# Performance work log

Hardware: AMD Instinct MI355X
Metric: run time of the kernel (lower is better)

Reference implementation:

```python
import jax, jax.numpy as jnp
import numpy as np

NUM_TNETS = 8388608
NUM_PINS = 20971520
NUM_NODES = 1048576

def setup_inputs() -> dict:
    key = jax.random.key(0)
    k1, k2, k3 = jax.random.split(key, 3)
    beta = jax.random.uniform(k1, (1,), dtype=jnp.float32)
    tnet_weights = jax.random.uniform(k2, (NUM_TNETS,), dtype=jnp.float32)
    flat_tnet2pin = jax.random.randint(k3, (2 * NUM_TNETS,), 0, NUM_PINS, dtype=jnp.int64)
    pin2node_map = jax.random.randint(jax.random.fold_in(key, 7), (NUM_PINS,), 0, NUM_NODES, dtype=jnp.int64)
    return {
        "beta": beta,
        "tnet_weights": tnet_weights,
        "flat_tnet2pin": flat_tnet2pin,
        "pin2node_map": pin2node_map,
    }

def reference(beta, tnet_weights, flat_tnet2pin, pin2node_map):
    # flat_tnet2pin layout: [src_0, dst_0, src_1, dst_1, ...] (2 pins per timing arc)
    # gather node id for every arc pin: [2*num_tnets]
    node_idx = pin2node_map[flat_tnet2pin]
    # each arc's weight is added at both its source and sink node
    w = jnp.repeat(tnet_weights, 2)  # [w0, w0, w1, w1, ...] matches flat layout
    out = jnp.zeros(NUM_NODES, dtype=jnp.float32).at[node_idx].add(w)
    return out * beta
```

## Files before the change

kernel.cpp:

```cpp
#include <hip/hip_runtime.h>
#include <stdint.h>


#define TILE 4096
#define THREADS 512
#define IPT  8
#define NB1  160
#define SHIFT1 17
#define CAP1 114688
#define TILES_PER_BIN1 28
#define NB2  256
#define SHIFT2 12
#define CAP2 81920
#define ACC_NODES 4096
#define CTRL_BYTES 8192

typedef unsigned long long item_t;
typedef int   int4_ev   __attribute__((ext_vector_type(4)));
typedef float float4_ev __attribute__((ext_vector_type(4)));
typedef unsigned long long ull2_ev __attribute__((ext_vector_type(2)));

__device__ __forceinline__ item_t pack_item(uint32_t key, float w) {
    return (item_t)key | ((item_t)__float_as_uint(w) << 32);
}

__device__ __forceinline__ void multisplit_flush(
    uint32_t (&key)[IPT], float (&wv)[IPT], int (&bin)[IPT],
    int tile_cnt, int shift,
    int* __restrict__ gcur, item_t* __restrict__ gout, size_t cap)
{
    __shared__ int hist[256];
    __shared__ int basex[256];
    __shared__ int gbase[256];
    __shared__ int wsum[4];
    __shared__ item_t stage[TILE];
    const int t = threadIdx.x;

    if (t < 256) hist[t] = 0;
    __syncthreads();

    int rank[IPT];
#pragma unroll
    for (int k = 0; k < IPT; ++k)
        rank[k] = (bin[k] >= 0) ? atomicAdd(&hist[bin[k]], 1) : 0;
    __syncthreads();

    int val = (t < 256) ? hist[t] : 0;
    int inc = val;
#pragma unroll
    for (int d = 1; d < 64; d <<= 1) {
        int n = __shfl_up(inc, d, 64);
        if ((t & 63) >= d) inc += n;
    }
    if (t < 256 && (t & 63) == 63) wsum[t >> 6] = inc;
    __syncthreads();
    if (t < 256) {
        int w = t >> 6, prefix = 0;
        if (w > 0) prefix += wsum[0];
        if (w > 1) prefix += wsum[1];
        if (w > 2) prefix += wsum[2];
        basex[t] = prefix + inc - val;
        gbase[t] = (val > 0) ? atomicAdd(&gcur[t], val) : 0;
    }
    __syncthreads();

#pragma unroll
    for (int k = 0; k < IPT; ++k) {
        if (bin[k] >= 0)
            stage[basex[bin[k]] + rank[k]] = pack_item(key[k], wv[k]);
    }
    __syncthreads();

    for (int j = t; j < tile_cnt; j += THREADS) {
        item_t e = stage[j];
        int b = (int)((uint32_t)(e & 0xffffffffull) >> shift);
        long long dst = (long long)gbase[b] + (j - basex[b]);
        if (dst >= 0 && dst < (long long)cap)
            __builtin_nontemporal_store(e, &gout[(size_t)b * cap + (size_t)dst]);
    }
}

__global__ __launch_bounds__(THREADS, 8) void k1_partition_pins(
    const int* __restrict__ flat_pins, const float* __restrict__ weights,
    int* __restrict__ cur1, item_t* __restrict__ items1, int total)
{
    const int tileBase = blockIdx.x * TILE;
    const int t = threadIdx.x;
    const int base = tileBase + t * IPT;
    uint32_t key[IPT]; float wv[IPT]; int bin[IPT];

    if (base + IPT <= total) {
        int4_ev   p[2];
        float4_ev w;
#pragma unroll
        for (int v = 0; v < 2; ++v)
            p[v] = __builtin_nontemporal_load((const int4_ev*)(flat_pins + base) + v);
        w = __builtin_nontemporal_load((const float4_ev*)(weights + (base >> 1)));
#pragma unroll
        for (int k = 0; k < IPT; ++k) {
            int pin = p[k >> 2][k & 3];
            key[k] = (uint32_t)pin;
            wv[k]  = w[(k >> 1) & 3];
            bin[k] = pin >> SHIFT1;
        }
    } else {
#pragma unroll
        for (int k = 0; k < IPT; ++k) {
            int i = base + k;
            bool ok = i < total;
            int pin = ok ? flat_pins[i] : 0;
            key[k] = (uint32_t)pin;
            wv[k]  = ok ? weights[i >> 1] : 0.f;
            bin[k] = ok ? (pin >> SHIFT1) : -1;
        }
    }
    int cnt = min(TILE, total - tileBase);
    multisplit_flush(key, wv, bin, cnt, SHIFT1, cur1, items1, (size_t)CAP1);
}

__global__ __launch_bounds__(THREADS, 8) void k2_gather_partition(
    const item_t* __restrict__ items1, const int* __restrict__ cur1,
    const int* __restrict__ pin2node,
    int* __restrict__ cur2, item_t* __restrict__ items2)
{
    const int q = blockIdx.x;
    const int r = q & 7;
    const int s = q >> 3;
    const int bin  = r + 8 * (s / TILES_PER_BIN1);
    const int tile = s % TILES_PER_BIN1;
    const int cnt = min(cur1[bin], (int)CAP1);
    const int tbase = tile * TILE;
    if (tbase >= cnt) return;

    const item_t* src = items1 + (size_t)bin * CAP1;
    const int t = threadIdx.x;
    const int base = tbase + t * IPT;
    uint32_t key[IPT]; float wv[IPT]; int b2[IPT];

    if (base + IPT <= cnt) {
        ull2_ev it[4];
#pragma unroll
        for (int v = 0; v < 4; ++v)
            it[v] = __builtin_nontemporal_load((const ull2_ev*)(src + base) + v);
#pragma unroll
        for (int k = 0; k < IPT; ++k) {
            item_t e = it[k >> 1][k & 1];
            int node = pin2node[(uint32_t)(e & 0xffffffffull)];
            key[k] = (uint32_t)node;
            wv[k]  = __uint_as_float((uint32_t)(e >> 32));
            b2[k]  = node >> SHIFT2;
        }
    } else {
#pragma unroll
        for (int k = 0; k < IPT; ++k) {
            int i = base + k;
            bool ok = i < cnt;
            item_t e = ok ? src[i] : 0ull;
            int node = ok ? pin2node[(uint32_t)(e & 0xffffffffull)] : 0;
            key[k] = (uint32_t)node;
            wv[k]  = __uint_as_float((uint32_t)(e >> 32));
            b2[k]  = ok ? (node >> SHIFT2) : -1;
        }
    }
    int tcnt = min(TILE, cnt - tbase);
    multisplit_flush(key, wv, b2, tcnt, SHIFT2, cur2, items2, (size_t)CAP2);
}

__global__ __launch_bounds__(1024) void k3_accumulate(
    const item_t* __restrict__ items2, const int* __restrict__ cur2,
    const float* __restrict__ beta, float* __restrict__ out, int num_nodes)
{
    __shared__ float acc[ACC_NODES];
    const int b = blockIdx.x;
    const int t = threadIdx.x;
    for (int i = t; i < ACC_NODES; i += 1024) acc[i] = 0.f;
    __syncthreads();
    const int cnt = min(cur2[b], (int)CAP2);
    const item_t* src = items2 + (size_t)b * CAP2;
    for (int i = t; i < cnt; i += 1024) {
        item_t it = __builtin_nontemporal_load(&src[i]);
        atomicAdd(&acc[(uint32_t)(it & 0xffffffffull) & (ACC_NODES - 1)],
                  __uint_as_float((uint32_t)(it >> 32)));
    }
    __syncthreads();
    const float bt = beta[0];
    const int nodeBase = b << SHIFT2;
    for (int i = t; i < ACC_NODES; i += 1024) {
        int n = nodeBase + i;
        if (n < num_nodes) out[n] = acc[i] * bt;
    }
}

__global__ __launch_bounds__(256) void scatter_device(
    const float* __restrict__ beta, const float* __restrict__ tnet_weights,
    const long long* __restrict__ pin_pairs, const int* __restrict__ pin2node_map,
    float* __restrict__ out, int num_tnets)
{
    int t = blockIdx.x * blockDim.x + threadIdx.x;
    if (t >= num_tnets) return;
    long long pp = pin_pairs[t];
    float w = tnet_weights[t] * beta[0];
    atomicAdd(&out[pin2node_map[(int)(pp & 0xffffffffLL)]], w);
    atomicAdd(&out[pin2node_map[(int)(pp >> 32)]], w);
}

extern "C" void kernel_launch(void* const* d_in, const int* in_sizes, int n_in,
                              void* d_out, int out_size, void* d_ws, size_t ws_size,
                              hipStream_t stream) {
    const float* beta         = (const float*)d_in[0];
    const float* weights      = (const float*)d_in[1];
    const int*   flat_pins    = (const int*)d_in[2];
    const int*   pin2node     = (const int*)d_in[3];
    float* out = (float*)d_out;

    const int num_tnets = in_sizes[1];
    const int total     = in_sizes[2];
    const int num_nodes = out_size;

    const size_t items1Bytes = (size_t)NB1 * CAP1 * sizeof(item_t);
    const size_t items2Bytes = (size_t)NB2 * CAP2 * sizeof(item_t);

    int* cur1 = (int*)d_ws;
    int* cur2 = (int*)((char*)d_ws + 2048);
    const int gridTiles = (total + TILE - 1) / TILE;

    if (ws_size >= CTRL_BYTES + items1Bytes + items2Bytes) {
        item_t* items1 = (item_t*)((char*)d_ws + CTRL_BYTES);
        item_t* items2 = (item_t*)((char*)d_ws + CTRL_BYTES + items1Bytes);
        (void)hipMemsetAsync(d_ws, 0, CTRL_BYTES, stream);
        k1_partition_pins<<<gridTiles, THREADS, 0, stream>>>(
            flat_pins, weights, cur1, items1, total);
        k2_gather_partition<<<NB1 * TILES_PER_BIN1, THREADS, 0, stream>>>(
            items1, cur1, pin2node, cur2, items2);
        k3_accumulate<<<NB2, 1024, 0, stream>>>(items2, cur2, beta, out, num_nodes);
    } else {
        (void)hipMemsetAsync(d_out, 0, (size_t)out_size * sizeof(float), stream);
        scatter_device<<<(num_tnets + 255) / 256, 256, 0, stream>>>(
            beta, weights, (const long long*)flat_pins, pin2node, out, num_tnets);
    }
}
```

Before: 483.6 us.

## Replace second partition pass with per-XCD global atomic partial sums

```diff
diff --git a/kernel.cpp b/kernel.cpp
--- a/kernel.cpp
+++ b/kernel.cpp
@@ -9,10 +9,7 @@
 #define SHIFT1 17
 #define CAP1 114688
 #define TILES_PER_BIN1 28
-#define NB2  256
-#define SHIFT2 12
-#define CAP2 81920
-#define ACC_NODES 4096
+#define NXCD 8
 #define CTRL_BYTES 8192
 
 typedef unsigned long long item_t;
@@ -118,10 +115,10 @@
     multisplit_flush(key, wv, bin, cnt, SHIFT1, cur1, items1, (size_t)CAP1);
 }
 
-__global__ __launch_bounds__(THREADS, 8) void k2_gather_partition(
+__global__ __launch_bounds__(THREADS, 8) void k2_gather_atomic(
     const item_t* __restrict__ items1, const int* __restrict__ cur1,
     const int* __restrict__ pin2node,
-    int* __restrict__ cur2, item_t* __restrict__ items2)
+    float* __restrict__ part, int num_nodes)
 {
     const int q = blockIdx.x;
     const int r = q & 7;
@@ -132,10 +129,10 @@
     const int tbase = tile * TILE;
     if (tbase >= cnt) return;
 
+    float* __restrict__ dst = part + (size_t)r * (size_t)num_nodes;
     const item_t* src = items1 + (size_t)bin * CAP1;
     const int t = threadIdx.x;
     const int base = tbase + t * IPT;
-    uint32_t key[IPT]; float wv[IPT]; int b2[IPT];
 
     if (base + IPT <= cnt) {
         ull2_ev it[4];
@@ -146,48 +143,45 @@
         for (int k = 0; k < IPT; ++k) {
             item_t e = it[k >> 1][k & 1];
             int node = pin2node[(uint32_t)(e & 0xffffffffull)];
-            key[k] = (uint32_t)node;
-            wv[k]  = __uint_as_float((uint32_t)(e >> 32));
-            b2[k]  = node >> SHIFT2;
+            atomicAdd(&dst[node], __uint_as_float((uint32_t)(e >> 32)));
         }
     } else {
 #pragma unroll
         for (int k = 0; k < IPT; ++k) {
             int i = base + k;
-            bool ok = i < cnt;
-            item_t e = ok ? src[i] : 0ull;
-            int node = ok ? pin2node[(uint32_t)(e & 0xffffffffull)] : 0;
-            key[k] = (uint32_t)node;
-            wv[k]  = __uint_as_float((uint32_t)(e >> 32));
-            b2[k]  = ok ? (node >> SHIFT2) : -1;
-        }
-    }
-    int tcnt = min(TILE, cnt - tbase);
-    multisplit_flush(key, wv, b2, tcnt, SHIFT2, cur2, items2, (size_t)CAP2);
-}
-
-__global__ __launch_bounds__(1024) void k3_accumulate(
-    const item_t* __restrict__ items2, const int* __restrict__ cur2,
-    const float* __restrict__ beta, float* __restrict__ out, int num_nodes)
-{
-    __shared__ float acc[ACC_NODES];
-    const int b = blockIdx.x;
-    const int t = threadIdx.x;
-    for (int i = t; i < ACC_NODES; i += 1024) acc[i] = 0.f;
-    __syncthreads();
-    const int cnt = min(cur2[b], (int)CAP2);
-    const item_t* src = items2 + (size_t)b * CAP2;
-    for (int i = t; i < cnt; i += 1024) {
-        item_t it = __builtin_nontemporal_load(&src[i]);
-        atomicAdd(&acc[(uint32_t)(it & 0xffffffffull) & (ACC_NODES - 1)],
-                  __uint_as_float((uint32_t)(it >> 32)));
-    }
-    __syncthreads();
+            if (i < cnt) {
+                item_t e = src[i];
+                int node = pin2node[(uint32_t)(e & 0xffffffffull)];
+                atomicAdd(&dst[node], __uint_as_float((uint32_t)(e >> 32)));
+            }
+        }
+    }
+}
+
+__global__ __launch_bounds__(256) void k3_reduce(
+    const float* __restrict__ part, const float* __restrict__ beta,
+    float* __restrict__ out, int num_nodes)
+{
     const float bt = beta[0];
-    const int nodeBase = b << SHIFT2;
-    for (int i = t; i < ACC_NODES; i += 1024) {
-        int n = nodeBase + i;
-        if (n < num_nodes) out[n] = acc[i] * bt;
+    const int i4 = blockIdx.x * 256 + threadIdx.x;
+    const int n = i4 * 4;
+    if (n + 3 < num_nodes) {
+        float4_ev s = {0.f, 0.f, 0.f, 0.f};
+#pragma unroll
+        for (int x = 0; x < NXCD; ++x)
+            s += *(const float4_ev*)(part + (size_t)x * (size_t)num_nodes + n);
+        *(float4_ev*)(out + n) = s * bt;
+    } else {
+        for (int k = 0; k < 4; ++k) {
+            int nn = n + k;
+            if (nn < num_nodes) {
+                float s = 0.f;
+#pragma unroll
+                for (int x = 0; x < NXCD; ++x)
+                    s += part[(size_t)x * (size_t)num_nodes + nn];
+                out[nn] = s * bt;
+            }
+        }
     }
 }
 
@@ -218,21 +212,23 @@
     const int num_nodes = out_size;
 
     const size_t items1Bytes = (size_t)NB1 * CAP1 * sizeof(item_t);
-    const size_t items2Bytes = (size_t)NB2 * CAP2 * sizeof(item_t);
+    const size_t partBytes   = (size_t)NXCD * (size_t)num_nodes * sizeof(float);
 
     int* cur1 = (int*)d_ws;
-    int* cur2 = (int*)((char*)d_ws + 2048);
     const int gridTiles = (total + TILE - 1) / TILE;
 
-    if (ws_size >= CTRL_BYTES + items1Bytes + items2Bytes) {
+    if (ws_size >= CTRL_BYTES + items1Bytes + partBytes) {
         item_t* items1 = (item_t*)((char*)d_ws + CTRL_BYTES);
-        item_t* items2 = (item_t*)((char*)d_ws + CTRL_BYTES + items1Bytes);
+        float*  part   = (float*)((char*)d_ws + CTRL_BYTES + items1Bytes);
         (void)hipMemsetAsync(d_ws, 0, CTRL_BYTES, stream);
+        (void)hipMemsetAsync(part, 0, partBytes, stream);
         k1_partition_pins<<<gridTiles, THREADS, 0, stream>>>(
             flat_pins, weights, cur1, items1, total);
-        k2_gather_partition<<<NB1 * TILES_PER_BIN1, THREADS, 0, stream>>>(
-            items1, cur1, pin2node, cur2, items2);
-        k3_accumulate<<<NB2, 1024, 0, stream>>>(items2, cur2, beta, out, num_nodes);
+        k2_gather_atomic<<<NB1 * TILES_PER_BIN1, THREADS, 0, stream>>>(
+            items1, cur1, pin2node, part, num_nodes);
+        const int i4slots = (num_nodes + 3) / 4;
+        k3_reduce<<<(i4slots + 255) / 256, 256, 0, stream>>>(
+            part, beta, out, num_nodes);
     } else {
         (void)hipMemsetAsync(d_out, 0, (size_t)out_size * sizeof(float), stream);
         scatter_device<<<(num_tnets + 255) / 256, 256, 0, stream>>>(
```

Result: slower. 1.084 ms (+124.1%).

## Fuse pin2node gather into first partition pass and drop pin-bucketing stage

Applied to the files above, without the earlier changes.

```diff
diff --git a/kernel.cpp b/kernel.cpp
--- a/kernel.cpp
+++ b/kernel.cpp
@@ -5,10 +5,6 @@
 #define TILE 4096
 #define THREADS 512
 #define IPT  8
-#define NB1  160
-#define SHIFT1 17
-#define CAP1 114688
-#define TILES_PER_BIN1 28
 #define NB2  256
 #define SHIFT2 12
 #define CAP2 81920
@@ -80,9 +76,10 @@
     }
 }
 
-__global__ __launch_bounds__(THREADS, 8) void k1_partition_pins(
+__global__ __launch_bounds__(THREADS, 8) void k1_gather_split(
     const int* __restrict__ flat_pins, const float* __restrict__ weights,
-    int* __restrict__ cur1, item_t* __restrict__ items1, int total)
+    const int* __restrict__ pin2node,
+    int* __restrict__ cur2, item_t* __restrict__ items2, int total)
 {
     const int tileBase = blockIdx.x * TILE;
     const int t = threadIdx.x;
@@ -96,77 +93,32 @@
         for (int v = 0; v < 2; ++v)
             p[v] = __builtin_nontemporal_load((const int4_ev*)(flat_pins + base) + v);
         w = __builtin_nontemporal_load((const float4_ev*)(weights + (base >> 1)));
+        int node[IPT];
+#pragma unroll
+        for (int k = 0; k < IPT; ++k)
+            node[k] = pin2node[(uint32_t)p[k >> 2][k & 3]];
 #pragma unroll
         for (int k = 0; k < IPT; ++k) {
-            int pin = p[k >> 2][k & 3];
-            key[k] = (uint32_t)pin;
+            key[k] = (uint32_t)node[k];
             wv[k]  = w[(k >> 1) & 3];
-            bin[k] = pin >> SHIFT1;
+            bin[k] = node[k] >> SHIFT2;
         }
     } else {
 #pragma unroll
         for (int k = 0; k < IPT; ++k) {
             int i = base + k;
             bool ok = i < total;
-            int pin = ok ? flat_pins[i] : 0;
-            key[k] = (uint32_t)pin;
+            int node = ok ? pin2node[(uint32_t)flat_pins[i]] : 0;
+            key[k] = (uint32_t)node;
             wv[k]  = ok ? weights[i >> 1] : 0.f;
-            bin[k] = ok ? (pin >> SHIFT1) : -1;
+            bin[k] = ok ? (node >> SHIFT2) : -1;
         }
     }
     int cnt = min(TILE, total - tileBase);
-    multisplit_flush(key, wv, bin, cnt, SHIFT1, cur1, items1, (size_t)CAP1);
-}
-
-__global__ __launch_bounds__(THREADS, 8) void k2_gather_partition(
-    const item_t* __restrict__ items1, const int* __restrict__ cur1,
-    const int* __restrict__ pin2node,
-    int* __restrict__ cur2, item_t* __restrict__ items2)
-{
-    const int q = blockIdx.x;
-    const int r = q & 7;
-    const int s = q >> 3;
-    const int bin  = r + 8 * (s / TILES_PER_BIN1);
-    const int tile = s % TILES_PER_BIN1;
-    const int cnt = min(cur1[bin], (int)CAP1);
-    const int tbase = tile * TILE;
-    if (tbase >= cnt) return;
-
-    const item_t* src = items1 + (size_t)bin * CAP1;
-    const int t = threadIdx.x;
-    const int base = tbase + t * IPT;
-    uint32_t key[IPT]; float wv[IPT]; int b2[IPT];
-
-    if (base + IPT <= cnt) {
-        ull2_ev it[4];
-#pragma unroll
-        for (int v = 0; v < 4; ++v)
-            it[v] = __builtin_nontemporal_load((const ull2_ev*)(src + base) + v);
-#pragma unroll
-        for (int k = 0; k < IPT; ++k) {
-            item_t e = it[k >> 1][k & 1];
-            int node = pin2node[(uint32_t)(e & 0xffffffffull)];
-            key[k] = (uint32_t)node;
-            wv[k]  = __uint_as_float((uint32_t)(e >> 32));
-            b2[k]  = node >> SHIFT2;
-        }
-    } else {
-#pragma unroll
-        for (int k = 0; k < IPT; ++k) {
-            int i = base + k;
-            bool ok = i < cnt;
-            item_t e = ok ? src[i] : 0ull;
-            int node = ok ? pin2node[(uint32_t)(e & 0xffffffffull)] : 0;
-            key[k] = (uint32_t)node;
-            wv[k]  = __uint_as_float((uint32_t)(e >> 32));
-            b2[k]  = ok ? (node >> SHIFT2) : -1;
-        }
-    }
-    int tcnt = min(TILE, cnt - tbase);
-    multisplit_flush(key, wv, b2, tcnt, SHIFT2, cur2, items2, (size_t)CAP2);
-}
-
-__global__ __launch_bounds__(1024) void k3_accumulate(
+    multisplit_flush(key, wv, bin, cnt, SHIFT2, cur2, items2, (size_t)CAP2);
+}
+
+__global__ __launch_bounds__(1024) void k2_accumulate(
     const item_t* __restrict__ items2, const int* __restrict__ cur2,
     const float* __restrict__ beta, float* __restrict__ out, int num_nodes)
 {
@@ -177,10 +129,25 @@
     __syncthreads();
     const int cnt = min(cur2[b], (int)CAP2);
     const item_t* src = items2 + (size_t)b * CAP2;
-    for (int i = t; i < cnt; i += 1024) {
-        item_t it = __builtin_nontemporal_load(&src[i]);
-        atomicAdd(&acc[(uint32_t)(it & 0xffffffffull) & (ACC_NODES - 1)],
-                  __uint_as_float((uint32_t)(it >> 32)));
+
+    const int nvec = cnt >> 2;
+    for (int g = t; g < nvec; g += 1024) {
+        const item_t* p = src + ((size_t)g << 2);
+        ull2_ev a0 = __builtin_nontemporal_load((const ull2_ev*)p);
+        ull2_ev a1 = __builtin_nontemporal_load((const ull2_ev*)p + 1);
+#pragma unroll
+        for (int k = 0; k < 2; ++k) {
+            item_t e0 = a0[k], e1 = a1[k];
+            atomicAdd(&acc[(uint32_t)(e0 & 0xffffffffull) & (ACC_NODES - 1)],
+                      __uint_as_float((uint32_t)(e0 >> 32)));
+            atomicAdd(&acc[(uint32_t)(e1 & 0xffffffffull) & (ACC_NODES - 1)],
+                      __uint_as_float((uint32_t)(e1 >> 32)));
+        }
+    }
+    for (int i = (nvec << 2) + t; i < cnt; i += 1024) {
+        item_t e = __builtin_nontemporal_load(&src[i]);
+        atomicAdd(&acc[(uint32_t)(e & 0xffffffffull) & (ACC_NODES - 1)],
+                  __uint_as_float((uint32_t)(e >> 32)));
     }
     __syncthreads();
     const float bt = beta[0];
@@ -217,22 +184,17 @@
     const int total     = in_sizes[2];
     const int num_nodes = out_size;
 
-    const size_t items1Bytes = (size_t)NB1 * CAP1 * sizeof(item_t);
     const size_t items2Bytes = (size_t)NB2 * CAP2 * sizeof(item_t);
 
-    int* cur1 = (int*)d_ws;
-    int* cur2 = (int*)((char*)d_ws + 2048);
+    int* cur2 = (int*)d_ws;
     const int gridTiles = (total + TILE - 1) / TILE;
 
-    if (ws_size >= CTRL_BYTES + items1Bytes + items2Bytes) {
-        item_t* items1 = (item_t*)((char*)d_ws + CTRL_BYTES);
-        item_t* items2 = (item_t*)((char*)d_ws + CTRL_BYTES + items1Bytes);
+    if (ws_size >= CTRL_BYTES + items2Bytes) {
+        item_t* items2 = (item_t*)((char*)d_ws + CTRL_BYTES);
         (void)hipMemsetAsync(d_ws, 0, CTRL_BYTES, stream);
-        k1_partition_pins<<<gridTiles, THREADS, 0, stream>>>(
-            flat_pins, weights, cur1, items1, total);
-        k2_gather_partition<<<NB1 * TILES_PER_BIN1, THREADS, 0, stream>>>(
-            items1, cur1, pin2node, cur2, items2);
-        k3_accumulate<<<NB2, 1024, 0, stream>>>(items2, cur2, beta, out, num_nodes);
+        k1_gather_split<<<gridTiles, THREADS, 0, stream>>>(
+            flat_pins, weights, pin2node, cur2, items2, total);
+        k2_accumulate<<<NB2, 1024, 0, stream>>>(items2, cur2, beta, out, num_nodes);
     } else {
         (void)hipMemsetAsync(d_out, 0, (size_t)out_size * sizeof(float), stream);
         scatter_device<<<(num_tnets + 255) / 256, 256, 0, stream>>>(
```

Measured after the change: 590.3 us. 1.22x slower.

## Coarsen radix bins and split accumulation into partial blocks plus reduce

Applied to the files above, without the earlier changes.

```diff
diff --git a/kernel.cpp b/kernel.cpp
--- a/kernel.cpp
+++ b/kernel.cpp
@@ -5,14 +5,16 @@
 #define TILE 4096
 #define THREADS 512
 #define IPT  8
-#define NB1  160
-#define SHIFT1 17
-#define CAP1 114688
-#define TILES_PER_BIN1 28
-#define NB2  256
-#define SHIFT2 12
-#define CAP2 81920
-#define ACC_NODES 4096
+#define NB1  40
+#define SHIFT1 19
+#define CAP1 430080
+#define TPB1 105
+#define NB2  64
+#define SHIFT2 14
+#define CAP2 270336
+#define ACC_NODES 16384
+#define PARTS 8
+#define CHK (CAP2 / PARTS)
 #define CTRL_BYTES 8192
 
 typedef unsigned long long item_t;
@@ -126,8 +128,8 @@
     const int q = blockIdx.x;
     const int r = q & 7;
     const int s = q >> 3;
-    const int bin  = r + 8 * (s / TILES_PER_BIN1);
-    const int tile = s % TILES_PER_BIN1;
+    const int bin  = r + 8 * (s / TPB1);
+    const int tile = s % TPB1;
     const int cnt = min(cur1[bin], (int)CAP1);
     const int tbase = tile * TILE;
     if (tbase >= cnt) return;
@@ -166,28 +168,75 @@
     multisplit_flush(key, wv, b2, tcnt, SHIFT2, cur2, items2, (size_t)CAP2);
 }
 
-__global__ __launch_bounds__(1024) void k3_accumulate(
+__global__ __launch_bounds__(1024, 8) void k3_accumulate_part(
     const item_t* __restrict__ items2, const int* __restrict__ cur2,
-    const float* __restrict__ beta, float* __restrict__ out, int num_nodes)
+    float* __restrict__ partials)
 {
     __shared__ float acc[ACC_NODES];
-    const int b = blockIdx.x;
+    const int b = blockIdx.x >> 3;
+    const int p = blockIdx.x & (PARTS - 1);
     const int t = threadIdx.x;
     for (int i = t; i < ACC_NODES; i += 1024) acc[i] = 0.f;
     __syncthreads();
+
     const int cnt = min(cur2[b], (int)CAP2);
+    const int lo  = p * CHK;
+    const int hi  = min(cnt, lo + CHK);
     const item_t* src = items2 + (size_t)b * CAP2;
-    for (int i = t; i < cnt; i += 1024) {
-        item_t it = __builtin_nontemporal_load(&src[i]);
-        atomicAdd(&acc[(uint32_t)(it & 0xffffffffull) & (ACC_NODES - 1)],
-                  __uint_as_float((uint32_t)(it >> 32)));
-    }
-    __syncthreads();
+
+    const int nv = (hi > lo) ? ((hi - lo) >> 2) : 0;
+    for (int g = t; g < nv; g += 1024) {
+        const item_t* pp = src + lo + ((size_t)g << 2);
+        ull2_ev a0 = __builtin_nontemporal_load((const ull2_ev*)pp);
+        ull2_ev a1 = __builtin_nontemporal_load((const ull2_ev*)pp + 1);
+#pragma unroll
+        for (int k = 0; k < 2; ++k) {
+            item_t e0 = a0[k], e1 = a1[k];
+            atomicAdd(&acc[(uint32_t)(e0 & 0xffffffffull) & (ACC_NODES - 1)],
+                      __uint_as_float((uint32_t)(e0 >> 32)));
+            atomicAdd(&acc[(uint32_t)(e1 & 0xffffffffull) & (ACC_NODES - 1)],
+                      __uint_as_float((uint32_t)(e1 >> 32)));
+        }
+    }
+    for (int i = lo + (nv << 2) + t; i < hi; i += 1024) {
+        item_t e = __builtin_nontemporal_load(&src[i]);
+        atomicAdd(&acc[(uint32_t)(e & 0xffffffffull) & (ACC_NODES - 1)],
+                  __uint_as_float((uint32_t)(e >> 32)));
+    }
+    __syncthreads();
+
+    float* __restrict__ dst = partials + (size_t)blockIdx.x * ACC_NODES;
+    for (int i = t; i < ACC_NODES; i += 1024) dst[i] = acc[i];
+}
+
+__global__ __launch_bounds__(256) void k4_reduce(
+    const float* __restrict__ partials, const float* __restrict__ beta,
+    float* __restrict__ out, int num_nodes)
+{
     const float bt = beta[0];
-    const int nodeBase = b << SHIFT2;
-    for (int i = t; i < ACC_NODES; i += 1024) {
-        int n = nodeBase + i;
-        if (n < num_nodes) out[n] = acc[i] * bt;
+    const int n = (blockIdx.x * 256 + threadIdx.x) << 2;
+    if (n + 3 < num_nodes) {
+        const int b   = n >> SHIFT2;
+        const int off = n & (ACC_NODES - 1);
+        const float* base = partials + ((size_t)b * PARTS) * ACC_NODES + off;
+        float4_ev s = {0.f, 0.f, 0.f, 0.f};
+#pragma unroll
+        for (int p = 0; p < PARTS; ++p)
+            s += *(const float4_ev*)(base + (size_t)p * ACC_NODES);
+        *(float4_ev*)(out + n) = s * bt;
+    } else {
+        for (int k = 0; k < 4; ++k) {
+            int nn = n + k;
+            if (nn < num_nodes) {
+                const int b   = nn >> SHIFT2;
+                const int off = nn & (ACC_NODES - 1);
+                float s = 0.f;
+#pragma unroll
+                for (int p = 0; p < PARTS; ++p)
+                    s += partials[((size_t)b * PARTS + p) * ACC_NODES + off];
+                out[nn] = s * bt;
+            }
+        }
     }
 }
 
@@ -219,20 +268,26 @@
 
     const size_t items1Bytes = (size_t)NB1 * CAP1 * sizeof(item_t);
     const size_t items2Bytes = (size_t)NB2 * CAP2 * sizeof(item_t);
+    const size_t partBytes   = (size_t)NB2 * PARTS * ACC_NODES * sizeof(float);
 
     int* cur1 = (int*)d_ws;
     int* cur2 = (int*)((char*)d_ws + 2048);
     const int gridTiles = (total + TILE - 1) / TILE;
 
-    if (ws_size >= CTRL_BYTES + items1Bytes + items2Bytes) {
+    if (ws_size >= CTRL_BYTES + items1Bytes + items2Bytes + partBytes) {
         item_t* items1 = (item_t*)((char*)d_ws + CTRL_BYTES);
         item_t* items2 = (item_t*)((char*)d_ws + CTRL_BYTES + items1Bytes);
+        float*  partials = (float*)((char*)d_ws + CTRL_BYTES + items1Bytes + items2Bytes);
         (void)hipMemsetAsync(d_ws, 0, CTRL_BYTES, stream);
         k1_partition_pins<<<gridTiles, THREADS, 0, stream>>>(
             flat_pins, weights, cur1, items1, total);
-        k2_gather_partition<<<NB1 * TILES_PER_BIN1, THREADS, 0, stream>>>(
+        k2_gather_partition<<<NB1 * TPB1, THREADS, 0, stream>>>(
             items1, cur1, pin2node, cur2, items2);
-        k3_accumulate<<<NB2, 1024, 0, stream>>>(items2, cur2, beta, out, num_nodes);
+        k3_accumulate_part<<<NB2 * PARTS, 1024, 0, stream>>>(
+            items2, cur2, partials);
+        const int i4slots = (num_nodes + 3) / 4;
+        k4_reduce<<<(i4slots + 255) / 256, 256, 0, stream>>>(
+            partials, beta, out, num_nodes);
     } else {
         (void)hipMemsetAsync(d_out, 0, (size_t)out_size * sizeof(float), stream);
         scatter_device<<<(num_tnets + 255) / 256, 256, 0, stream>>>(
```

Measured after the change: 452.3 us. 6.5% less time.
